# Kernel optimization log

Hardware: AMD Instinct MI355X
Metric: run time of the kernel (lower is better)

Reference implementation:

```python
import jax, jax.numpy as jnp
import numpy as np

C = 256        # in_channels
HEADS = 8
HD = 64        # dim_heads
INNER = HEADS * HD   # 512
G = 32         # norm_groups
FF = 4 * INNER # 2048
EPS = 1e-5


def setup_inputs() -> dict:
    key = jax.random.key(0)
    ks = jax.random.split(key, 12)
    r = lambda k, shp: jax.random.normal(k, shp, jnp.float32) * 0.02
    return {
        "x": jax.random.normal(ks[0], (1, C, 16, 16, 16), jnp.float32),
        "gn_g": jnp.ones((C,), jnp.float32),
        "gn_b": jnp.zeros((C,), jnp.float32),
        "w_in": r(ks[1], (INNER, C)),   # Conv3d 1x1x1 as (out,in) matrix
        "b_in": jnp.zeros((INNER,), jnp.float32),
        "wq": r(ks[2], (INNER, INNER)),
        "wk": r(ks[3], (INNER, INNER)),
        "wv": r(ks[4], (INNER, INNER)),
        "ln1_g": jnp.ones((INNER,), jnp.float32),
        "ln1_b": jnp.zeros((INNER,), jnp.float32),
        "ff_w1": r(ks[5], (FF, INNER)),
        "ff_b1": jnp.zeros((FF,), jnp.float32),
        "ff_w2": r(ks[6], (INNER, FF)),
        "ff_b2": jnp.zeros((INNER,), jnp.float32),
        "ln2_g": jnp.ones((INNER,), jnp.float32),
        "ln2_b": jnp.zeros((INNER,), jnp.float32),
        "w_out": r(ks[7], (C, INNER)),  # Conv3d 1x1x1 back to C
        "b_out": jnp.zeros((C,), jnp.float32),
    }


def _group_norm(x, g, b):
    # x: (B,C,D,H,W), G groups, normalize over (C//G, D, H, W)
    B, Cc, D, H, W = x.shape
    xr = x.reshape(B, G, Cc // G, D, H, W)
    mu = jnp.mean(xr, axis=(2, 3, 4, 5), keepdims=True)
    var = jnp.var(xr, axis=(2, 3, 4, 5), keepdims=True)
    xr = (xr - mu) * jax.lax.rsqrt(var + EPS)
    xn = xr.reshape(B, Cc, D, H, W)
    return xn * g[None, :, None, None, None] + b[None, :, None, None, None]


def _layer_norm(x, g, b):
    mu = jnp.mean(x, axis=-1, keepdims=True)
    var = jnp.var(x, axis=-1, keepdims=True)
    return (x - mu) * jax.lax.rsqrt(var + EPS) * g + b


def reference(x, gn_g, gn_b, w_in, b_in, wq, wk, wv, ln1_g, ln1_b,
              ff_w1, ff_b1, ff_w2, ff_b2, ln2_g, ln2_b, w_out, b_out):
    B, Cc, D, H, W = x.shape
    x_in = x
    # GroupNorm + proj_in (1x1x1 conv == channel matmul)
    h = _group_norm(x, gn_g, gn_b)
    t = jnp.einsum('bcdhw,oc->bodhw', h, w_in) + b_in[None, :, None, None, None]
    N = D * H * W
    t = t.reshape(B, INNER, N).transpose(0, 2, 1)  # (B, N, INNER)

    # self-attention (manual einsum softmax einsum)
    q = (t @ wq.T).reshape(B, N, HEADS, HD)
    k = (t @ wk.T).reshape(B, N, HEADS, HD)
    v = (t @ wv.T).reshape(B, N, HEADS, HD)
    scale = HD ** (-0.5)
    scores = jnp.einsum('bihd,bjhd->bhij', q, k) * scale  # (B,H,N,N)
    attn = jax.nn.softmax(scores, axis=-1)
    o = jnp.einsum('bhij,bjhd->bihd', attn, v).reshape(B, N, INNER)
    # out_proj is Identity (q_dim == inner_dim), dropout=0
    t = _layer_norm(o + t, ln1_g, ln1_b)

    # FeedForward: Linear -> GELU (erf) -> Linear
    ff = jax.nn.gelu(t @ ff_w1.T + ff_b1, approximate=False) @ ff_w2.T + ff_b2
    t = _layer_norm(ff + t, ln2_g, ln2_b)

    # proj_out + residual
    y = t.transpose(0, 2, 1).reshape(B, INNER, D, H, W)
    out = jnp.einsum('bidhw,oi->bodhw', y, w_out) + b_out[None, :, None, None, None]
    return out + x_in
```

## Files before the change

### kernel.cpp

```cpp
#include <hip/hip_runtime.h>
#include <hip/hip_bf16.h>

typedef unsigned short u16;
typedef __attribute__((ext_vector_type(8))) short short8;
typedef __attribute__((ext_vector_type(4))) float floatx4;

#define LOG2E 1.44269504088896f
#define CEXP (0.125f * LOG2E)

static __device__ __forceinline__ u16 f2b(float f) {
  union { float f; unsigned u; } v; v.f = f;
  unsigned r = v.u + 0x7fffu + ((v.u >> 16) & 1u);
  return (u16)(r >> 16);
}
static __device__ __forceinline__ float b2f(u16 b) {
  union { float f; unsigned u; } v; v.u = ((unsigned)b) << 16;
  return v.f;
}
static __device__ __forceinline__ void async16(const u16* g, u16* l) {
  __builtin_amdgcn_global_load_lds(
      (const __attribute__((address_space(1))) unsigned int*)g,
      (__attribute__((address_space(3))) unsigned int*)l, 16, 0, 0);
}
static __device__ __forceinline__ float fexp2(float x) {
  return __builtin_amdgcn_exp2f(x);
}

__global__ __launch_bounds__(256) void f2b_all(
    const float* __restrict__ s0, const float* __restrict__ s1, const float* __restrict__ s2,
    const float* __restrict__ s3, const float* __restrict__ s4, const float* __restrict__ s5,
    const float* __restrict__ s6, const float* __restrict__ x,
    u16* __restrict__ d_win, u16* __restrict__ d_qkv, u16* __restrict__ d_f1,
    u16* __restrict__ d_f2, u16* __restrict__ d_wout, float2* __restrict__ cstats) {
  if (blockIdx.x >= 12288) {
    int c = blockIdx.x - 12288;
    const float4* p4 = (const float4*)(x + (size_t)c * 4096);
    float s = 0.f, ss = 0.f;
#pragma unroll
    for (int j = 0; j < 4; j++) {
      float4 v = p4[j * 256 + threadIdx.x];
      s += v.x + v.y + v.z + v.w;
      ss += v.x * v.x + v.y * v.y + v.z * v.z + v.w * v.w;
    }
    for (int m = 1; m < 64; m <<= 1) { s += __shfl_xor(s, m); ss += __shfl_xor(ss, m); }
    __shared__ float sb[8];
    int w = threadIdx.x >> 6;
    if ((threadIdx.x & 63) == 0) { sb[w * 2] = s; sb[w * 2 + 1] = ss; }
    __syncthreads();
    if (threadIdx.x == 0)
      cstats[c] = float2{sb[0] + sb[2] + sb[4] + sb[6], sb[1] + sb[3] + sb[5] + sb[7]};
    return;
  }
  int i = blockIdx.x * 256 + threadIdx.x;
  if (i < 131072) { d_win[i] = f2b(s0[i]); return; }
  i -= 131072;
  if (i < 262144) { d_qkv[i] = f2b(s1[i]); return; }
  i -= 262144;
  if (i < 262144) { d_qkv[262144 + i] = f2b(s2[i]); return; }
  i -= 262144;
  if (i < 262144) { d_qkv[524288 + i] = f2b(s3[i]); return; }
  i -= 262144;
  if (i < 1048576) { d_f1[i] = f2b(s4[i]); return; }
  i -= 1048576;
  if (i < 1048576) { d_f2[i] = f2b(s5[i]); return; }
  i -= 1048576;
  d_wout[i] = f2b(s6[i]);
}

__global__ __launch_bounds__(256) void gn_apply(const float* __restrict__ x, const float2* __restrict__ cstats,
                                                const float* __restrict__ gg, const float* __restrict__ gb,
                                                u16* __restrict__ hn) {
  int idx = blockIdx.x * 256 + threadIdx.x;
  int c = idx >> 12, n = idx & 4095;
  int g = c >> 3;
  float s = 0.f, ss = 0.f;
#pragma unroll
  for (int j = 0; j < 8; j++) {
    float2 p = cstats[g * 8 + j];
    s += p.x; ss += p.y;
  }
  float mu = s / 32768.f;
  float rs = rsqrtf(ss / 32768.f - mu * mu + 1e-5f);
  float v = (x[idx] - mu) * rs * gg[c] + gb[c];
  hn[(size_t)n * 256 + c] = f2b(v);
}

#define FLAG_BIAS 1
#define FLAG_GELU 2
#define FLAG_C32 4
#define FLAG_C16 8
#define FLAG_QKV 16
#define FLAG_FINAL 32

__global__ __launch_bounds__(256) void gemm_bt(
    const u16* __restrict__ A, const u16* __restrict__ B, const float* __restrict__ bias,
    float* __restrict__ C32, u16* __restrict__ C16, u16* __restrict__ C16b,
    u16* __restrict__ C16T, const float* __restrict__ resid,
    int M, int N, int K, int flags) {
  __shared__ u16 As[128 * 64];
  __shared__ u16 Bs[64 * 64];
  const int t = threadIdx.x;
  const int lane = t & 63;
  const int w = t >> 6;
  const int ln = lane & 15;
  const int quad = lane >> 4;
  const int m0 = blockIdx.x * 128;
  const int n0 = blockIdx.y * 64;
  const int wm = (w >> 1) * 64;
  const int wn = (w & 1) * 32;

  floatx4 acc[4][2];
#pragma unroll
  for (int i = 0; i < 4; i++)
#pragma unroll
    for (int j = 0; j < 2; j++) acc[i][j] = floatx4{0.f, 0.f, 0.f, 0.f};

  for (int k0 = 0; k0 < K; k0 += 64) {
    __syncthreads();
#pragma unroll
    for (int i = 0; i < 4; ++i) {
      int s = i * 256 + t;
      int row = s >> 3;
      int kb = (s & 7) ^ (row & 7);
      async16(A + (size_t)(m0 + row) * K + k0 + kb * 8, &As[(i * 256 + (t & ~63)) * 8]);
    }
#pragma unroll
    for (int i = 0; i < 2; ++i) {
      int s = i * 256 + t;
      int row = s >> 3;
      int kb = (s & 7) ^ (row & 7);
      async16(B + (size_t)(n0 + row) * K + k0 + kb * 8, &Bs[(i * 256 + (t & ~63)) * 8]);
    }
    __syncthreads();
#pragma unroll
    for (int ksi = 0; ksi < 2; ksi++) {
      short8 af[4], bfr[2];
      int kb = ksi * 4 + quad;
#pragma unroll
      for (int i = 0; i < 4; i++) {
        int m = wm + i * 16 + ln;
        af[i] = *(const short8*)&As[(m * 8 + (kb ^ (m & 7))) * 8];
      }
#pragma unroll
      for (int j = 0; j < 2; j++) {
        int n = wn + j * 16 + ln;
        bfr[j] = *(const short8*)&Bs[(n * 8 + (kb ^ (n & 7))) * 8];
      }
#pragma unroll
      for (int i = 0; i < 4; i++)
#pragma unroll
        for (int j = 0; j < 2; j++)
          acc[i][j] = __builtin_amdgcn_mfma_f32_16x16x32_bf16(af[i], bfr[j], acc[i][j], 0, 0, 0);
    }
  }

#pragma unroll
  for (int i = 0; i < 4; i++) {
#pragma unroll
    for (int j = 0; j < 2; j++) {
      int n = n0 + wn + j * 16 + ln;
      float bv = (flags & FLAG_BIAS) ? bias[n] : 0.f;
#pragma unroll
      for (int r = 0; r < 4; r++) {
        int m = m0 + wm + i * 16 + quad * 4 + r;
        float v = acc[i][j][r] + bv;
        if (flags & FLAG_GELU) v = 0.5f * v * (1.f + erff(v * 0.70710678118f));
        if (flags & FLAG_C32) C32[(size_t)m * N + n] = v;
        if (flags & FLAG_C16) C16[(size_t)m * N + n] = f2b(v);
        if (flags & FLAG_QKV) {
          if (n < 512) C16[(size_t)m * 512 + n] = f2b(v);
          else if (n < 1024) C16b[(size_t)m * 512 + (n - 512)] = f2b(v);
          else C16T[(size_t)(n - 1024) * M + m] = f2b(v);
        }
        if (flags & FLAG_FINAL)
          C32[(size_t)m * N + n] = v + bias[m] + resid[(size_t)m * N + n];
      }
    }
  }
}

__global__ __launch_bounds__(256) void gemm_ff1(
    const u16* __restrict__ A, const u16* __restrict__ B, const float* __restrict__ bias,
    u16* __restrict__ C16, int M, int N, int K) {
  __shared__ u16 As[128 * 64];
  __shared__ u16 Bs[128 * 64];
  const int t = threadIdx.x;
  const int lane = t & 63;
  const int w = t >> 6;
  const int ln = lane & 15;
  const int quad = lane >> 4;
  const int m0 = blockIdx.x * 128;
  const int n0 = blockIdx.y * 128;
  const int wm = (w >> 1) * 64;
  const int wn = (w & 1) * 64;

  floatx4 acc[4][4];
#pragma unroll
  for (int i = 0; i < 4; i++)
#pragma unroll
    for (int j = 0; j < 4; j++) acc[i][j] = floatx4{0.f, 0.f, 0.f, 0.f};

  for (int k0 = 0; k0 < K; k0 += 64) {
    __syncthreads();
#pragma unroll
    for (int i = 0; i < 4; ++i) {
      int s = i * 256 + t;
      int row = s >> 3;
      int kb = (s & 7) ^ (row & 7);
      async16(A + (size_t)(m0 + row) * K + k0 + kb * 8, &As[(i * 256 + (t & ~63)) * 8]);
      async16(B + (size_t)(n0 + row) * K + k0 + kb * 8, &Bs[(i * 256 + (t & ~63)) * 8]);
    }
    __syncthreads();
#pragma unroll
    for (int ksi = 0; ksi < 2; ksi++) {
      short8 af[4], bfr[4];
      int kb = ksi * 4 + quad;
#pragma unroll
      for (int i = 0; i < 4; i++) {
        int m = wm + i * 16 + ln;
        af[i] = *(const short8*)&As[(m * 8 + (kb ^ (m & 7))) * 8];
        int n = wn + i * 16 + ln;
        bfr[i] = *(const short8*)&Bs[(n * 8 + (kb ^ (n & 7))) * 8];
      }
#pragma unroll
      for (int i = 0; i < 4; i++)
#pragma unroll
        for (int j = 0; j < 4; j++)
          acc[i][j] = __builtin_amdgcn_mfma_f32_16x16x32_bf16(af[i], bfr[j], acc[i][j], 0, 0, 0);
    }
  }
#pragma unroll
  for (int i = 0; i < 4; i++)
#pragma unroll
    for (int j = 0; j < 4; j++) {
      int n = n0 + wn + j * 16 + ln;
      float bv = bias[n];
#pragma unroll
      for (int r = 0; r < 4; r++) {
        int m = m0 + wm + i * 16 + quad * 4 + r;
        float v = acc[i][j][r] + bv;
        v = 0.5f * v * (1.f + erff(v * 0.70710678118f));
        C16[(size_t)m * N + n] = f2b(v);
      }
    }
}

__global__ __launch_bounds__(256, 4) void attn_kernel(
    const u16* __restrict__ Q, const u16* __restrict__ Km, const u16* __restrict__ VT,
    u16* __restrict__ Opart, float* __restrict__ ML, int Nseq, int kvLen) {
  __shared__ u16 Ks[64 * 64];
  __shared__ u16 Vs[64 * 64];
  __shared__ u16 Ps[4 * 32 * 64];
  const int t = threadIdx.x;
  const int lane = t & 63;
  const int w = t >> 6;
  const int ln = lane & 15;
  const int quad = lane >> 4;
  const int h = blockIdx.y;
  const int q0 = blockIdx.x * 128;
  const int split = blockIdx.z;
  const int kvbase = split * kvLen;
  u16* Opw = Opart + (size_t)split * Nseq * 512;
  u16* Pw = &Ps[w * 32 * 64];

  short8 qf[2][2];
#pragma unroll
  for (int qt = 0; qt < 2; qt++)
#pragma unroll
    for (int ksi = 0; ksi < 2; ksi++)
      qf[qt][ksi] = *(const short8*)&Q[(size_t)(q0 + w * 32 + qt * 16 + ln) * 512 + h * 64 + ksi * 32 + quad * 8];

  floatx4 accO[2][4];
#pragma unroll
  for (int qt = 0; qt < 2; qt++)
#pragma unroll
    for (int td = 0; td < 4; td++) accO[qt][td] = floatx4{0.f, 0.f, 0.f, 0.f};
  float lsum[2] = {0.f, 0.f};

  for (int kv = 0; kv < kvLen; kv += 64) {
    const int kv0 = kvbase + kv;
    __syncthreads();
#pragma unroll
    for (int i = 0; i < 2; ++i) {
      int s = i * 256 + t;
      int row = s >> 3;
      int kb = (s & 7) ^ (row & 7);
      async16(Km + (size_t)(kv0 + row) * 512 + h * 64 + kb * 8, &Ks[(i * 256 + (t & ~63)) * 8]);
      async16(VT + (size_t)(h * 64 + row) * Nseq + kv0 + kb * 8, &Vs[(i * 256 + (t & ~63)) * 8]);
    }
    __syncthreads();

    floatx4 accS[2][4];
#pragma unroll
    for (int qt = 0; qt < 2; qt++)
#pragma unroll
      for (int tj = 0; tj < 4; tj++) accS[qt][tj] = floatx4{0.f, 0.f, 0.f, 0.f};
#pragma unroll
    for (int ksi = 0; ksi < 2; ksi++) {
      int kb = ksi * 4 + quad;
      short8 kf[4];
#pragma unroll
      for (int tj = 0; tj < 4; tj++) {
        int key = tj * 16 + ln;
        kf[tj] = *(const short8*)&Ks[(key * 8 + (kb ^ (key & 7))) * 8];
      }
#pragma unroll
      for (int qt = 0; qt < 2; qt++)
#pragma unroll
        for (int tj = 0; tj < 4; tj++)
          accS[qt][tj] = __builtin_amdgcn_mfma_f32_16x16x32_bf16(kf[tj], qf[qt][ksi], accS[qt][tj], 0, 0, 0);
    }

#pragma unroll
    for (int qt = 0; qt < 2; qt++) {
      int q8 = (qt * 16 + ln) * 8;
#pragma unroll
      for (int tj = 0; tj < 4; tj++) {
        float p0 = fexp2(accS[qt][tj][0] * CEXP);
        float p1 = fexp2(accS[qt][tj][1] * CEXP);
        float p2 = fexp2(accS[qt][tj][2] * CEXP);
        float p3 = fexp2(accS[qt][tj][3] * CEXP);
        lsum[qt] += (p0 + p1) + (p2 + p3);
        __hip_bfloat162 a01 = __float22bfloat162_rn(float2{p0, p1});
        __hip_bfloat162 a23 = __float22bfloat162_rn(float2{p2, p3});
        uint2 pk;
        pk.x = *(unsigned*)&a01;
        pk.y = *(unsigned*)&a23;
        int kbx = tj * 2 + (quad >> 1);
        *(uint2*)&Pw[(q8 + (kbx ^ (ln & 7))) * 8 + (quad & 1) * 4] = pk;
      }
    }

#pragma unroll
    for (int ksi = 0; ksi < 2; ksi++) {
      int kb = ksi * 4 + quad;
      short8 pf[2];
#pragma unroll
      for (int qt = 0; qt < 2; qt++)
        pf[qt] = *(const short8*)&Pw[((qt * 16 + ln) * 8 + (kb ^ (ln & 7))) * 8];
#pragma unroll
      for (int td = 0; td < 4; td++) {
        int d = td * 16 + ln;
        short8 vf = *(const short8*)&Vs[(d * 8 + (kb ^ (d & 7))) * 8];
#pragma unroll
        for (int qt = 0; qt < 2; qt++)
          accO[qt][td] = __builtin_amdgcn_mfma_f32_16x16x32_bf16(vf, pf[qt], accO[qt][td], 0, 0, 0);
      }
    }
  }

#pragma unroll
  for (int qt = 0; qt < 2; qt++) {
    lsum[qt] += __shfl_xor(lsum[qt], 16);
    lsum[qt] += __shfl_xor(lsum[qt], 32);
  }
#pragma unroll
  for (int qt = 0; qt < 2; qt++) {
    int q = q0 + w * 32 + qt * 16 + ln;
#pragma unroll
    for (int td = 0; td < 4; td++) {
      __hip_bfloat162 p01 = __float22bfloat162_rn(float2{accO[qt][td][0], accO[qt][td][1]});
      __hip_bfloat162 p23 = __float22bfloat162_rn(float2{accO[qt][td][2], accO[qt][td][3]});
      uint2 pk;
      pk.x = *(unsigned*)&p01;
      pk.y = *(unsigned*)&p23;
      *(uint2*)&Opw[(size_t)q * 512 + h * 64 + td * 16 + quad * 4] = pk;
    }
    if (quad == 0)
      ML[((size_t)split * 8 + h) * Nseq + q] = lsum[qt];
  }
}

__global__ __launch_bounds__(256) void ln_attn(
    const u16* __restrict__ Opart, const float* __restrict__ ML,
    const float* __restrict__ t32, const float* __restrict__ g, const float* __restrict__ be,
    float* __restrict__ o32, u16* __restrict__ o16) {
  int row = blockIdx.x;
  int t = threadIdx.x;
  float v[2];
#pragma unroll
  for (int p = 0; p < 2; p++) {
    int c = t + p * 256;
    int h = c >> 6;
    float lt = 0.f, acc = 0.f;
#pragma unroll
    for (int s = 0; s < 4; s++) {
      lt += ML[((size_t)s * 8 + h) * 4096 + row];
      acc += b2f(Opart[(size_t)s * 4096 * 512 + (size_t)row * 512 + c]);
    }
    v[p] = acc / lt + t32[(size_t)row * 512 + c];
  }
  float s = v[0] + v[1], ss = v[0] * v[0] + v[1] * v[1];
  for (int m = 1; m < 64; m <<= 1) { s += __shfl_xor(s, m); ss += __shfl_xor(ss, m); }
  __shared__ float sb[8];
  int w = t >> 6;
  if ((t & 63) == 0) { sb[w * 2] = s; sb[w * 2 + 1] = ss; }
  __syncthreads();
  s = sb[0] + sb[2] + sb[4] + sb[6];
  ss = sb[1] + sb[3] + sb[5] + sb[7];
  float mu = s / 512.f;
  float var = ss / 512.f - mu * mu;
  float rs = rsqrtf(var + 1e-5f);
#pragma unroll
  for (int p = 0; p < 2; p++) {
    int c = t + p * 256;
    float r0 = (v[p] - mu) * rs * g[c] + be[c];
    o32[(size_t)row * 512 + c] = r0;
    o16[(size_t)row * 512 + c] = f2b(r0);
  }
}

__global__ __launch_bounds__(256) void ln2k(
    const float* __restrict__ a, const float* __restrict__ b,
    const float* __restrict__ g, const float* __restrict__ be, u16* __restrict__ o16) {
  int row = blockIdx.x;
  int t = threadIdx.x;
  size_t base = (size_t)row * 512;
  float v0 = a[base + t] + b[base + t];
  float v1 = a[base + t + 256] + b[base + t + 256];
  float s = v0 + v1, ss = v0 * v0 + v1 * v1;
  for (int m = 1; m < 64; m <<= 1) { s += __shfl_xor(s, m); ss += __shfl_xor(ss, m); }
  __shared__ float sb[8];
  int w = t >> 6;
  if ((t & 63) == 0) { sb[w * 2] = s; sb[w * 2 + 1] = ss; }
  __syncthreads();
  s = sb[0] + sb[2] + sb[4] + sb[6];
  ss = sb[1] + sb[3] + sb[5] + sb[7];
  float mu = s / 512.f;
  float var = ss / 512.f - mu * mu;
  float rs = rsqrtf(var + 1e-5f);
  o16[base + t] = f2b((v0 - mu) * rs * g[t] + be[t]);
  o16[base + t + 256] = f2b((v1 - mu) * rs * g[t + 256] + be[t + 256]);
}

extern "C" void kernel_launch(void* const* d_in, const int* in_sizes, int n_in,
                              void* d_out, int out_size, void* d_ws, size_t ws_size,
                              hipStream_t stream) {
  const float* x = (const float*)d_in[0];
  const float* gn_g = (const float*)d_in[1];
  const float* gn_b = (const float*)d_in[2];
  const float* w_in = (const float*)d_in[3];
  const float* b_in = (const float*)d_in[4];
  const float* wq = (const float*)d_in[5];
  const float* wk = (const float*)d_in[6];
  const float* wv = (const float*)d_in[7];
  const float* ln1_g = (const float*)d_in[8];
  const float* ln1_b = (const float*)d_in[9];
  const float* ff_w1 = (const float*)d_in[10];
  const float* ff_b1 = (const float*)d_in[11];
  const float* ff_w2 = (const float*)d_in[12];
  const float* ff_b2 = (const float*)d_in[13];
  const float* ln2_g = (const float*)d_in[14];
  const float* ln2_b = (const float*)d_in[15];
  const float* w_out = (const float*)d_in[16];
  const float* b_out = (const float*)d_in[17];
  float* out = (float*)d_out;
  char* ws = (char*)d_ws;

  u16* w_in16 = (u16*)(ws + 0);
  u16* wqkv16 = (u16*)(ws + 262144);
  u16* fw116 = (u16*)(ws + 1835008);
  u16* fw216 = (u16*)(ws + 3932160);
  u16* wout16 = (u16*)(ws + 6029312);
  float* t32 = (float*)(ws + 6291456);
  u16* t16 = (u16*)(ws + 14680064);
  u16* u16b = (u16*)(ws + 14680064);
  u16* qb = (u16*)(ws + 18874368);
  u16* kb = (u16*)(ws + 23068672);
  u16* vt = (u16*)(ws + 27262976);
  u16* opart = (u16*)(ws + 31457280);
  float* ml = (float*)(ws + 48234496);
  u16* hn = (u16*)(ws + 49283072);
  float2* cstats = (float2*)(ws + 51380224);
  float* u32b = (float*)(ws + 18874368);
  u16* g16 = (u16*)(ws + 31457280);
  float* z32 = (float*)(ws + 6291456);
  u16* zb = (u16*)(ws + 14680064);

  f2b_all<<<12544, 256, 0, stream>>>(w_in, wq, wk, wv, ff_w1, ff_w2, w_out, x,
                                     w_in16, wqkv16, fw116, fw216, wout16, cstats);
  gn_apply<<<4096, 256, 0, stream>>>(x, cstats, gn_g, gn_b, hn);

  gemm_bt<<<dim3(32, 8), 256, 0, stream>>>(hn, w_in16, b_in, t32, t16, nullptr, nullptr, nullptr,
                                           4096, 512, 256, FLAG_BIAS | FLAG_C32 | FLAG_C16);
  gemm_bt<<<dim3(32, 24), 256, 0, stream>>>(t16, wqkv16, nullptr, nullptr, qb, kb, vt, nullptr,
                                            4096, 1536, 512, FLAG_QKV);
  attn_kernel<<<dim3(32, 8, 4), 256, 0, stream>>>(qb, kb, vt, opart, ml, 4096, 1024);
  ln_attn<<<4096, 256, 0, stream>>>(opart, ml, t32, ln1_g, ln1_b, u32b, u16b);
  gemm_ff1<<<dim3(32, 16), 256, 0, stream>>>(u16b, fw116, ff_b1, g16, 4096, 2048, 512);
  gemm_bt<<<dim3(32, 8), 256, 0, stream>>>(g16, fw216, ff_b2, z32, nullptr, nullptr, nullptr, nullptr,
                                           4096, 512, 2048, FLAG_BIAS | FLAG_C32);
  ln2k<<<4096, 256, 0, stream>>>(z32, u32b, ln2_g, ln2_b, zb);
  gemm_bt<<<dim3(2, 64), 256, 0, stream>>>(wout16, zb, b_out, out, nullptr, nullptr, nullptr, x,
                                           256, 4096, 512, FLAG_FINAL);
}
```

Before: 261.4 us.

## Use 128x128 GEMM tiles for QKV and FF2 with split-K, fold softmax scale into Q

```diff
diff --git a/kernel.cpp b/kernel.cpp
--- a/kernel.cpp
+++ b/kernel.cpp
@@ -94,8 +94,7 @@
 
 __global__ __launch_bounds__(256) void gemm_bt(
     const u16* __restrict__ A, const u16* __restrict__ B, const float* __restrict__ bias,
-    float* __restrict__ C32, u16* __restrict__ C16, u16* __restrict__ C16b,
-    u16* __restrict__ C16T, const float* __restrict__ resid,
+    float* __restrict__ C32, u16* __restrict__ C16, const float* __restrict__ resid,
     int M, int N, int K, int flags) {
   __shared__ u16 As[128 * 64];
   __shared__ u16 Bs[64 * 64];
@@ -164,14 +163,8 @@
       for (int r = 0; r < 4; r++) {
         int m = m0 + wm + i * 16 + quad * 4 + r;
         float v = acc[i][j][r] + bv;
-        if (flags & FLAG_GELU) v = 0.5f * v * (1.f + erff(v * 0.70710678118f));
         if (flags & FLAG_C32) C32[(size_t)m * N + n] = v;
         if (flags & FLAG_C16) C16[(size_t)m * N + n] = f2b(v);
-        if (flags & FLAG_QKV) {
-          if (n < 512) C16[(size_t)m * 512 + n] = f2b(v);
-          else if (n < 1024) C16b[(size_t)m * 512 + (n - 512)] = f2b(v);
-          else C16T[(size_t)(n - 1024) * M + m] = f2b(v);
-        }
         if (flags & FLAG_FINAL)
           C32[(size_t)m * N + n] = v + bias[m] + resid[(size_t)m * N + n];
       }
@@ -179,9 +172,11 @@
   }
 }
 
-__global__ __launch_bounds__(256) void gemm_ff1(
+__global__ __launch_bounds__(256) void gemm_big(
     const u16* __restrict__ A, const u16* __restrict__ B, const float* __restrict__ bias,
-    u16* __restrict__ C16, int M, int N, int K) {
+    float* __restrict__ C32, float* __restrict__ C32b,
+    u16* __restrict__ C16, u16* __restrict__ C16b, u16* __restrict__ C16T,
+    int M, int N, int K, int flags) {
   __shared__ u16 As[128 * 64];
   __shared__ u16 Bs[128 * 64];
   const int t = threadIdx.x;
@@ -193,6 +188,8 @@
   const int n0 = blockIdx.y * 128;
   const int wm = (w >> 1) * 64;
   const int wn = (w & 1) * 64;
+  const int kper = K / gridDim.z;
+  const int kbeg = blockIdx.z * kper;
 
   floatx4 acc[4][4];
 #pragma unroll
@@ -200,7 +197,7 @@
 #pragma unroll
     for (int j = 0; j < 4; j++) acc[i][j] = floatx4{0.f, 0.f, 0.f, 0.f};
 
-  for (int k0 = 0; k0 < K; k0 += 64) {
+  for (int k0 = kbeg; k0 < kbeg + kper; k0 += 64) {
     __syncthreads();
 #pragma unroll
     for (int i = 0; i < 4; ++i) {
@@ -229,20 +226,29 @@
           acc[i][j] = __builtin_amdgcn_mfma_f32_16x16x32_bf16(af[i], bfr[j], acc[i][j], 0, 0, 0);
     }
   }
-#pragma unroll
-  for (int i = 0; i < 4; i++)
+
+  float* Cz = blockIdx.z ? C32b : C32;
+#pragma unroll
+  for (int i = 0; i < 4; i++) {
 #pragma unroll
     for (int j = 0; j < 4; j++) {
       int n = n0 + wn + j * 16 + ln;
-      float bv = bias[n];
+      float bv = ((flags & FLAG_BIAS) && blockIdx.z == 0) ? bias[n] : 0.f;
 #pragma unroll
       for (int r = 0; r < 4; r++) {
         int m = m0 + wm + i * 16 + quad * 4 + r;
         float v = acc[i][j][r] + bv;
-        v = 0.5f * v * (1.f + erff(v * 0.70710678118f));
-        C16[(size_t)m * N + n] = f2b(v);
-      }
-    }
+        if (flags & FLAG_GELU) v = 0.5f * v * (1.f + erff(v * 0.70710678118f));
+        if (flags & FLAG_C32) Cz[(size_t)m * N + n] = v;
+        if (flags & FLAG_C16) C16[(size_t)m * N + n] = f2b(v);
+        if (flags & FLAG_QKV) {
+          if (n < 512) C16[(size_t)m * 512 + n] = f2b(v * CEXP);
+          else if (n < 1024) C16b[(size_t)m * 512 + (n - 512)] = f2b(v);
+          else C16T[(size_t)(n - 1024) * M + m] = f2b(v);
+        }
+      }
+    }
+  }
 }
 
 __global__ __launch_bounds__(256, 4) void attn_kernel(
@@ -316,10 +322,10 @@
       int q8 = (qt * 16 + ln) * 8;
 #pragma unroll
       for (int tj = 0; tj < 4; tj++) {
-        float p0 = fexp2(accS[qt][tj][0] * CEXP);
-        float p1 = fexp2(accS[qt][tj][1] * CEXP);
-        float p2 = fexp2(accS[qt][tj][2] * CEXP);
-        float p3 = fexp2(accS[qt][tj][3] * CEXP);
+        float p0 = fexp2(accS[qt][tj][0]);
+        float p1 = fexp2(accS[qt][tj][1]);
+        float p2 = fexp2(accS[qt][tj][2]);
+        float p3 = fexp2(accS[qt][tj][3]);
         lsum[qt] += (p0 + p1) + (p2 + p3);
         __hip_bfloat162 a01 = __float22bfloat162_rn(float2{p0, p1});
         __hip_bfloat162 a23 = __float22bfloat162_rn(float2{p2, p3});
@@ -374,7 +380,7 @@
 __global__ __launch_bounds__(256) void ln_attn(
     const u16* __restrict__ Opart, const float* __restrict__ ML,
     const float* __restrict__ t32, const float* __restrict__ g, const float* __restrict__ be,
-    float* __restrict__ o32, u16* __restrict__ o16) {
+    u16* __restrict__ o16) {
   int row = blockIdx.x;
   int t = threadIdx.x;
   float v[2];
@@ -404,20 +410,18 @@
 #pragma unroll
   for (int p = 0; p < 2; p++) {
     int c = t + p * 256;
-    float r0 = (v[p] - mu) * rs * g[c] + be[c];
-    o32[(size_t)row * 512 + c] = r0;
-    o16[(size_t)row * 512 + c] = f2b(r0);
-  }
-}
-
-__global__ __launch_bounds__(256) void ln2k(
-    const float* __restrict__ a, const float* __restrict__ b,
+    o16[(size_t)row * 512 + c] = f2b((v[p] - mu) * rs * g[c] + be[c]);
+  }
+}
+
+__global__ __launch_bounds__(256) void ln3(
+    const float* __restrict__ a, const float* __restrict__ b, const u16* __restrict__ c16,
     const float* __restrict__ g, const float* __restrict__ be, u16* __restrict__ o16) {
   int row = blockIdx.x;
   int t = threadIdx.x;
   size_t base = (size_t)row * 512;
-  float v0 = a[base + t] + b[base + t];
-  float v1 = a[base + t + 256] + b[base + t + 256];
+  float v0 = a[base + t] + b[base + t] + b2f(c16[base + t]);
+  float v1 = a[base + t + 256] + b[base + t + 256] + b2f(c16[base + t + 256]);
   float s = v0 + v1, ss = v0 * v0 + v1 * v1;
   for (int m = 1; m < 64; m <<= 1) { s += __shfl_xor(s, m); ss += __shfl_xor(ss, m); }
   __shared__ float sb[8];
@@ -469,28 +473,29 @@
   u16* kb = (u16*)(ws + 23068672);
   u16* vt = (u16*)(ws + 27262976);
   u16* opart = (u16*)(ws + 31457280);
+  u16* g16 = (u16*)(ws + 31457280);
   float* ml = (float*)(ws + 48234496);
   u16* hn = (u16*)(ws + 49283072);
   float2* cstats = (float2*)(ws + 51380224);
-  float* u32b = (float*)(ws + 18874368);
-  u16* g16 = (u16*)(ws + 31457280);
-  float* z32 = (float*)(ws + 6291456);
-  u16* zb = (u16*)(ws + 14680064);
+  float* z32a = (float*)(ws + 6291456);
+  float* z32b = (float*)(ws + 18874368);
+  u16* zb = (u16*)(ws + 27262976);
 
   f2b_all<<<12544, 256, 0, stream>>>(w_in, wq, wk, wv, ff_w1, ff_w2, w_out, x,
                                      w_in16, wqkv16, fw116, fw216, wout16, cstats);
   gn_apply<<<4096, 256, 0, stream>>>(x, cstats, gn_g, gn_b, hn);
 
-  gemm_bt<<<dim3(32, 8), 256, 0, stream>>>(hn, w_in16, b_in, t32, t16, nullptr, nullptr, nullptr,
+  gemm_bt<<<dim3(32, 8), 256, 0, stream>>>(hn, w_in16, b_in, t32, t16, nullptr,
                                            4096, 512, 256, FLAG_BIAS | FLAG_C32 | FLAG_C16);
-  gemm_bt<<<dim3(32, 24), 256, 0, stream>>>(t16, wqkv16, nullptr, nullptr, qb, kb, vt, nullptr,
-                                            4096, 1536, 512, FLAG_QKV);
+  gemm_big<<<dim3(32, 12), 256, 0, stream>>>(t16, wqkv16, nullptr, nullptr, nullptr, qb, kb, vt,
+                                             4096, 1536, 512, FLAG_QKV);
   attn_kernel<<<dim3(32, 8, 4), 256, 0, stream>>>(qb, kb, vt, opart, ml, 4096, 1024);
-  ln_attn<<<4096, 256, 0, stream>>>(opart, ml, t32, ln1_g, ln1_b, u32b, u16b);
-  gemm_ff1<<<dim3(32, 16), 256, 0, stream>>>(u16b, fw116, ff_b1, g16, 4096, 2048, 512);
-  gemm_bt<<<dim3(32, 8), 256, 0, stream>>>(g16, fw216, ff_b2, z32, nullptr, nullptr, nullptr, nullptr,
-                                           4096, 512, 2048, FLAG_BIAS | FLAG_C32);
-  ln2k<<<4096, 256, 0, stream>>>(z32, u32b, ln2_g, ln2_b, zb);
-  gemm_bt<<<dim3(2, 64), 256, 0, stream>>>(wout16, zb, b_out, out, nullptr, nullptr, nullptr, x,
+  ln_attn<<<4096, 256, 0, stream>>>(opart, ml, t32, ln1_g, ln1_b, u16b);
+  gemm_big<<<dim3(32, 16), 256, 0, stream>>>(u16b, fw116, ff_b1, nullptr, nullptr, g16, nullptr, nullptr,
+                                             4096, 2048, 512, FLAG_BIAS | FLAG_GELU | FLAG_C16);
+  gemm_big<<<dim3(32, 4, 2), 256, 0, stream>>>(g16, fw216, ff_b2, z32a, z32b, nullptr, nullptr, nullptr,
+                                               4096, 512, 2048, FLAG_BIAS | FLAG_C32);
+  ln3<<<4096, 256, 0, stream>>>(z32a, z32b, u16b, ln2_g, ln2_b, zb);
+  gemm_bt<<<dim3(2, 64), 256, 0, stream>>>(wout16, zb, b_out, out, nullptr, x,
                                            256, 4096, 512, FLAG_FINAL);
 }
```

After: 264.4 us. No clear change (+1.1%).
